# Kernel optimization log

Measured on AMD Instinct MI355X. Metric: run time of the kernel, lower is better.

The kernel has to match this reference:

```python
import jax, jax.numpy as jnp
import numpy as np

STATE_DIM = 512
N_AGENTS = 16
N_ACTIONS = 32
EMBED = 512          # mixing_embed_dim
Q_IN = STATE_DIM + N_AGENTS * N_ACTIONS  # 1024 (coma_critic arch)
ROWS = 32768         # bs * ts = 64 * 512


def _linear_params(key, d_in, d_out):
    kw, kb = jax.random.split(key)
    bound = 1.0 / np.sqrt(d_in)
    W = jax.random.uniform(kw, (d_in, d_out), minval=-bound, maxval=bound, dtype=jnp.float32)
    b = jax.random.uniform(kb, (d_out,), minval=-bound, maxval=bound, dtype=jnp.float32)
    return W, b


def setup_inputs() -> dict:
    key = jax.random.key(0)
    ks = jax.random.split(key, 8)
    states = jax.random.normal(ks[0], (ROWS, STATE_DIM), dtype=jnp.float32)
    actions = jax.random.uniform(ks[1], (ROWS, N_AGENTS * N_ACTIONS), dtype=jnp.float32)
    Qw1, Qb1 = _linear_params(ks[2], Q_IN, EMBED)
    Qw2, Qb2 = _linear_params(ks[3], EMBED, EMBED)
    Qw3, Qb3 = _linear_params(ks[4], EMBED, 1)
    Vw1, Vb1 = _linear_params(ks[5], STATE_DIM, EMBED)
    Vw2, Vb2 = _linear_params(ks[6], EMBED, EMBED)
    Vw3, Vb3 = _linear_params(ks[7], EMBED, 1)
    return {
        "states": states, "actions": actions,
        "Qw1": Qw1, "Qb1": Qb1, "Qw2": Qw2, "Qb2": Qb2, "Qw3": Qw3, "Qb3": Qb3,
        "Vw1": Vw1, "Vb1": Vb1, "Vw2": Vw2, "Vb2": Vb2, "Vw3": Vw3, "Vb3": Vb3,
    }


def _mlp3(x, W1, b1, W2, b2, W3, b3):
    h = jax.nn.relu(x @ W1 + b1)
    h = jax.nn.relu(h @ W2 + b2)
    return h @ W3 + b3


def reference(states, actions,
              Qw1, Qb1, Qw2, Qb2, Qw3, Qb3,
              Vw1, Vb1, Vw2, Vb2, Vw3, Vb3):
    # coma_critic arch: inputs = cat([states, joint-action one-hots], dim=1)
    inputs = jnp.concatenate([states, actions], axis=1)  # [bs*ts, Q_IN]
    q_outputs = _mlp3(inputs, Qw1, Qb1, Qw2, Qb2, Qw3, Qb3)  # [bs*ts, 1]
    v_outputs = _mlp3(states, Vw1, Vb1, Vw2, Vb2, Vw3, Vb3)  # [bs*ts, 1]
    return q_outputs, v_outputs
```

## Files before the change

### kernel.cpp

```cpp
#include <hip/hip_runtime.h>


#define ROWS 32768
#define EMBED 512

using frag_ab = __attribute__((ext_vector_type(8))) short;
using f32x4   = __attribute__((ext_vector_type(4))) float;

__device__ __forceinline__ unsigned short f2bf(float f) {
    unsigned int u = __builtin_bit_cast(unsigned int, f);
    return (unsigned short)((u + 0x7fffu + ((u >> 16) & 1u)) >> 16);
}

__device__ __forceinline__ unsigned pk2rne(float lo, float hi) {
    return (unsigned)f2bf(lo) | ((unsigned)f2bf(hi) << 16);
}

__device__ __forceinline__ void async_copy16(const void* g, void* l) {
    __builtin_amdgcn_global_load_lds(
        (const __attribute__((address_space(1))) unsigned int*)g,
        (__attribute__((address_space(3))) unsigned int*)l, 16, 0, 0);
}

#define VM0()   asm volatile("s_waitcnt vmcnt(0)" ::: "memory")
#define LGKM0() asm volatile("s_waitcnt lgkmcnt(0)" ::: "memory")
#define SBAR()  __builtin_amdgcn_s_barrier()
#define SCHED0() __builtin_amdgcn_sched_barrier(0)

__global__ __launch_bounds__(256)
void prep(const float* __restrict__ states, const float* __restrict__ actions,
          const float* __restrict__ Qw1, const float* __restrict__ Qw2,
          const float* __restrict__ Vw1, const float* __restrict__ Vw2,
          const float* __restrict__ qb3, const float* __restrict__ vb3,
          unsigned short* __restrict__ X,
          unsigned short* __restrict__ Qw1t, unsigned short* __restrict__ Qw2t,
          unsigned short* __restrict__ Vw1t, unsigned short* __restrict__ Vw2t,
          float* __restrict__ out) {
    const int b = blockIdx.x, tid = threadIdx.x;
    if (b < 4096) {
        int c = b * 256 + tid;
        int m = c >> 5, col = (c & 31) * 32;
        const float* src = (col < 512) ? states + (size_t)m * 512 + col
                                       : actions + (size_t)m * 512 + (col - 512);
        float4 f[8];
#pragma unroll
        for (int i = 0; i < 8; i++) f[i] = ((const float4*)src)[i];
        uint4* dst = (uint4*)(X + (size_t)m * 1024 + col);
#pragma unroll
        for (int i = 0; i < 4; i++)
            dst[i] = make_uint4(pk2rne(f[2*i].x,   f[2*i].y),
                                pk2rne(f[2*i].z,   f[2*i].w),
                                pk2rne(f[2*i+1].x, f[2*i+1].y),
                                pk2rne(f[2*i+1].z, f[2*i+1].w));
    } else if (b < 4416) {
        __shared__ float T[64][65];
        int tg = b - 4096;
        const float* W; unsigned short* O; int Krows, kt, nt;
        if (tg < 128) { W = Qw1; O = Qw1t; Krows = 1024; kt = tg >> 3; nt = tg & 7; }
        else {
            tg -= 128; int seg = tg >> 6, r = tg & 63;
            kt = r >> 3; nt = r & 7; Krows = 512;
            W = (seg == 0) ? Qw2 : (seg == 1) ? Vw1 : Vw2;
            O = (seg == 0) ? Qw2t : (seg == 1) ? Vw1t : Vw2t;
        }
        const int k0 = kt * 64, n0 = nt * 64;
        const int rr = tid >> 4, c4 = (tid & 15) * 4;
#pragma unroll
        for (int p = 0; p < 4; ++p) {
            float4 v = *(const float4*)&W[(size_t)(k0 + p * 16 + rr) * 512 + n0 + c4];
            T[p * 16 + rr][c4]     = v.x;
            T[p * 16 + rr][c4 + 1] = v.y;
            T[p * 16 + rr][c4 + 2] = v.z;
            T[p * 16 + rr][c4 + 3] = v.w;
        }
        __syncthreads();
        const int n = tid >> 2, kc = (tid & 3) * 16;
        unsigned pk[8];
#pragma unroll
        for (int j = 0; j < 8; ++j)
            pk[j] = pk2rne(T[kc + 2 * j][n], T[kc + 2 * j + 1][n]);
        uint4* dst = (uint4*)(O + (size_t)(n0 + n) * Krows + k0 + kc);
        dst[0] = make_uint4(pk[0], pk[1], pk[2], pk[3]);
        dst[1] = make_uint4(pk[4], pk[5], pk[6], pk[7]);
    } else {
        int i = (b - 4416) * 256 + tid;
        out[i] = (i < ROWS) ? qb3[0] : vb3[0];
    }
}

__device__ __forceinline__ void gemm_256(
    const unsigned short* __restrict__ A, int ldaE,
    const unsigned short* __restrict__ Bt, int ldbE,
    int K, int bm, int bn, char* smb, f32x4 acc[8][4])
{
    const int tid = threadIdx.x, wave = tid >> 6, lane = tid & 63;
    const int im = wave >> 2, in = wave & 3;
    const int lrow = lane & 15, quad = lane >> 4;
    const int ldaB = ldaE * 2, ldbB = ldbE * 2;

    const int srow = wave * 8 + (lane >> 3);
    const int scol = (((lane & 7) ^ ((lane >> 3) & 7)) << 4);
    const char* gA = (const char*)A + (size_t)(bm + srow) * ldaB + scol;
    const char* gB = (const char*)Bt + (size_t)(bn + srow) * ldbB + scol;
    char* ldsAw = smb + wave * 1024;
    char* ldsBw = smb + 65536 + wave * 1024;

    auto stageA = [&](int b, int h) {
        const char* g = gA + (size_t)(h * 128) * ldaB;
        char* l = ldsAw + b * 32768 + h * 16384;
        async_copy16(g, l);
        async_copy16(g + (size_t)64 * ldaB, l + 8192);
    };
    auto stageB = [&](int b, int h) {
        const char* g = gB + (size_t)(h * 128) * ldbB;
        char* l = ldsBw + b * 32768 + h * 16384;
        async_copy16(g, l);
        async_copy16(g + (size_t)64 * ldbB, l + 8192);
    };

    frag_ab a[4][2], b0[2][2], b1[2][2];

    auto readA = [&](int b, int mh) {
        const char* base = smb + b * 32768 + im * 16384;
#pragma unroll
        for (int i = 0; i < 4; ++i) {
            const int r = mh * 64 + i * 16 + lrow;
#pragma unroll
            for (int s = 0; s < 2; ++s)
                a[i][s] = *(const frag_ab*)(base + r * 128 +
                              (((s * 4 + quad) ^ (r & 7)) << 4));
        }
    };
    auto readB = [&](int b, int nh, frag_ab bb[2][2]) {
#pragma unroll
        for (int j = 0; j < 2; ++j) {
            const int nr = in * 64 + nh * 32 + j * 16 + lrow;
            const char* base = smb + 65536 + b * 32768 + (nr >> 7) * 16384;
            const int r = nr & 127;
#pragma unroll
            for (int s = 0; s < 2; ++s)
                bb[j][s] = *(const frag_ab*)(base + r * 128 +
                               (((s * 4 + quad) ^ (r & 7)) << 4));
        }
    };
    auto mma = [&](int mh, int nh, frag_ab bb[2][2]) {
        __builtin_amdgcn_s_setprio(1);
#pragma unroll
        for (int s = 0; s < 2; ++s)
#pragma unroll
            for (int i = 0; i < 4; ++i)
#pragma unroll
                for (int j = 0; j < 2; ++j)
                    acc[mh * 4 + i][nh * 2 + j] =
                        __builtin_amdgcn_mfma_f32_16x16x32_bf16(
                            a[i][s], bb[j][s], acc[mh * 4 + i][nh * 2 + j],
                            0, 0, 0);
        __builtin_amdgcn_s_setprio(0);
    };

    stageA(0, 0); stageB(0, 0); stageB(0, 1); stageA(0, 1);
    gA += 128; gB += 128;
    VM0();
    SBAR();

    const int NT = K >> 6;
    int buf = 0;
    for (int t = 0; t < NT; ++t) {
        const bool more = (t + 1 < NT);
        const int nb = buf ^ 1;
        readA(buf, 0); readB(buf, 0, b0);
        if (more) { stageA(nb, 0); stageB(nb, 0); }
        SBAR(); LGKM0(); SCHED0();
        mma(0, 0, b0);
        SBAR();
        readB(buf, 1, b1);
        if (more) stageB(nb, 1);
        SBAR(); LGKM0(); SCHED0();
        mma(0, 1, b1);
        SBAR();
        readA(buf, 1);
        if (more) { stageA(nb, 1); gA += 128; gB += 128; }
        SBAR(); LGKM0(); SCHED0();
        mma(1, 1, b1);
        SBAR();
        SBAR(); LGKM0(); SCHED0();
        mma(1, 0, b0);
        if (more) VM0();
        SBAR();
        buf ^= 1;
    }
}

__device__ __forceinline__ void decode_work(int bid, int& mi, int& v) {
    int work = ((bid & 7) << 6) | (bid >> 3);
    mi = work >> 2; v = work & 3;
}

__global__ __launch_bounds__(512, 2)
void layer1(const unsigned short* __restrict__ X,
            const unsigned short* __restrict__ Qw1t,
            const unsigned short* __restrict__ Vw1t,
            const float* __restrict__ Qb1, const float* __restrict__ Vb1,
            unsigned short* __restrict__ h1Q, unsigned short* __restrict__ h1V) {
    __shared__ __align__(16) char smem[131072];
    int mi, v; decode_work(blockIdx.x, mi, v);
    const bool isV = v >= 2;
    const int bm = mi * 256, bn = (v & 1) * 256;
    const int K = isV ? 512 : 1024;
    const unsigned short* Wt = isV ? Vw1t : Qw1t;
    const float* bias = isV ? Vb1 : Qb1;
    unsigned short* H = isV ? h1V : h1Q;

    f32x4 acc[8][4] = {};
    gemm_256(X, 1024, Wt, K, K, bm, bn, smem, acc);

    const int tid = threadIdx.x, wave = tid >> 6, lane = tid & 63;
    const int im = wave >> 2, in = wave & 3;
    const int lrow = lane & 15, quad = lane >> 4;
#pragma unroll
    for (int j = 0; j < 4; ++j) {
        const int col = bn + in * 64 + j * 16 + lrow;
        const float bc = bias[col];
#pragma unroll
        for (int i = 0; i < 8; ++i) {
            const int row0 = bm + im * 128 + i * 16 + quad * 4;
#pragma unroll
            for (int r = 0; r < 4; ++r) {
                float val = acc[i][j][r] + bc;
                val = val > 0.0f ? val : 0.0f;
                H[(size_t)(row0 + r) * EMBED + col] = f2bf(val);
            }
        }
    }
}

__global__ __launch_bounds__(512, 2)
void layer2(const unsigned short* __restrict__ h1Q,
            const unsigned short* __restrict__ h1V,
            const unsigned short* __restrict__ Qw2t,
            const unsigned short* __restrict__ Vw2t,
            const float* __restrict__ Qb2, const float* __restrict__ Vb2,
            const float* __restrict__ Qw3, const float* __restrict__ Vw3,
            float* __restrict__ out) {
    __shared__ __align__(16) char smem[131072];
    int mi, v; decode_work(blockIdx.x, mi, v);
    const bool isV = v >= 2;
    const int bm = mi * 256, bn = (v & 1) * 256;
    const unsigned short* A  = isV ? h1V : h1Q;
    const unsigned short* Wt = isV ? Vw2t : Qw2t;
    const float* bias = isV ? Vb2 : Qb2;
    const float* w3   = isV ? Vw3 : Qw3;
    float* op = out + (isV ? ROWS : 0);

    f32x4 acc[8][4] = {};
    gemm_256(A, 512, Wt, 512, 512, bm, bn, smem, acc);

    const int tid = threadIdx.x, wave = tid >> 6, lane = tid & 63;
    const int im = wave >> 2, in = wave & 3;
    const int lrow = lane & 15, quad = lane >> 4;
    float bc[4], wc[4];
#pragma unroll
    for (int j = 0; j < 4; ++j) {
        const int col = bn + in * 64 + j * 16 + lrow;
        bc[j] = bias[col];
        wc[j] = w3[col];
    }
#pragma unroll
    for (int i = 0; i < 8; ++i) {
#pragma unroll
        for (int r = 0; r < 4; ++r) {
            float s = 0.0f;
#pragma unroll
            for (int j = 0; j < 4; ++j) {
                float val = acc[i][j][r] + bc[j];
                val = val > 0.0f ? val : 0.0f;
                s += val * wc[j];
            }
#pragma unroll
            for (int m = 1; m < 16; m <<= 1) s += __shfl_xor(s, m, 64);
            if (lrow == 0)
                atomicAdd(&op[bm + im * 128 + i * 16 + quad * 4 + r], s);
        }
    }
}

extern "C" void kernel_launch(void* const* d_in, const int* in_sizes, int n_in,
                              void* d_out, int out_size, void* d_ws, size_t ws_size,
                              hipStream_t stream) {
    const float* states  = (const float*)d_in[0];
    const float* actions = (const float*)d_in[1];
    const float* Qw1 = (const float*)d_in[2];
    const float* Qb1 = (const float*)d_in[3];
    const float* Qw2 = (const float*)d_in[4];
    const float* Qb2 = (const float*)d_in[5];
    const float* Qw3 = (const float*)d_in[6];
    const float* Qb3 = (const float*)d_in[7];
    const float* Vw1 = (const float*)d_in[8];
    const float* Vb1 = (const float*)d_in[9];
    const float* Vw2 = (const float*)d_in[10];
    const float* Vb2 = (const float*)d_in[11];
    const float* Vw3 = (const float*)d_in[12];
    const float* Vb3 = (const float*)d_in[13];
    float* out = (float*)d_out;

    char* ws = (char*)d_ws;
    unsigned short* X    = (unsigned short*)ws;
    unsigned short* h1Q  = (unsigned short*)(ws + 67108864);
    unsigned short* h1V  = (unsigned short*)(ws + 100663296);
    unsigned short* Qw1t = (unsigned short*)(ws + 134217728);
    unsigned short* Qw2t = Qw1t + 512 * 1024;
    unsigned short* Vw1t = Qw2t + 512 * 512;
    unsigned short* Vw2t = Vw1t + 512 * 512;

    prep<<<dim3(4672), dim3(256), 0, stream>>>(states, actions, Qw1, Qw2, Vw1, Vw2,
                                               Qb3, Vb3, X, Qw1t, Qw2t, Vw1t, Vw2t, out);

    layer1<<<dim3(512), dim3(512), 0, stream>>>(X, Qw1t, Vw1t, Qb1, Vb1, h1Q, h1V);
    layer2<<<dim3(512), dim3(512), 0, stream>>>(h1Q, h1V, Qw2t, Vw2t, Qb2, Vb2, Qw3, Vw3, out);
}
```

Measured before the change: 289.6 us.

## Restructure GEMM main loop to prefetch two tiles ahead with partial vmcnt waits

The GEMM inner loop moves from a fine-grained schedule, with several barriers and lgkmcnt waits interleaving staged half-tiles, to a simpler double-buffer scheme. Both buffers are staged up front, the loop waits with vmcnt(8) so only the current tile must have landed, runs all four MMA blocks back to back, then refills the just-consumed buffer two tiles ahead. Separately, the prep conversion kernel now has each thread handle 8 elements instead of 32, with four times as many blocks, to raise memory parallelism. The goal is fewer barriers and more load latency hidden behind compute. The cost is less interleaving of LDS reads with MFMAs within an iteration.

```diff
diff --git a/kernel.cpp b/kernel.cpp
--- a/kernel.cpp
+++ b/kernel.cpp
@@ -22,10 +22,9 @@
         (__attribute__((address_space(3))) unsigned int*)l, 16, 0, 0);
 }
 
+#define VM8()   asm volatile("s_waitcnt vmcnt(8)" ::: "memory")
 #define VM0()   asm volatile("s_waitcnt vmcnt(0)" ::: "memory")
-#define LGKM0() asm volatile("s_waitcnt lgkmcnt(0)" ::: "memory")
 #define SBAR()  __builtin_amdgcn_s_barrier()
-#define SCHED0() __builtin_amdgcn_sched_barrier(0)
 
 __global__ __launch_bounds__(256)
 void prep(const float* __restrict__ states, const float* __restrict__ actions,
@@ -37,24 +36,19 @@
           unsigned short* __restrict__ Vw1t, unsigned short* __restrict__ Vw2t,
           float* __restrict__ out) {
     const int b = blockIdx.x, tid = threadIdx.x;
-    if (b < 4096) {
-        int c = b * 256 + tid;
-        int m = c >> 5, col = (c & 31) * 32;
+    if (b < 16384) {
+        int g = b * 256 + tid;
+        int m = g >> 7, col = (g & 127) * 8;
         const float* src = (col < 512) ? states + (size_t)m * 512 + col
                                        : actions + (size_t)m * 512 + (col - 512);
-        float4 f[8];
-#pragma unroll
-        for (int i = 0; i < 8; i++) f[i] = ((const float4*)src)[i];
-        uint4* dst = (uint4*)(X + (size_t)m * 1024 + col);
-#pragma unroll
-        for (int i = 0; i < 4; i++)
-            dst[i] = make_uint4(pk2rne(f[2*i].x,   f[2*i].y),
-                                pk2rne(f[2*i].z,   f[2*i].w),
-                                pk2rne(f[2*i+1].x, f[2*i+1].y),
-                                pk2rne(f[2*i+1].z, f[2*i+1].w));
-    } else if (b < 4416) {
+        float4 f0 = ((const float4*)src)[0];
+        float4 f1 = ((const float4*)src)[1];
+        *(uint4*)(X + (size_t)m * 1024 + col) =
+            make_uint4(pk2rne(f0.x, f0.y), pk2rne(f0.z, f0.w),
+                       pk2rne(f1.x, f1.y), pk2rne(f1.z, f1.w));
+    } else if (b < 16704) {
         __shared__ float T[64][65];
-        int tg = b - 4096;
+        int tg = b - 16384;
         const float* W; unsigned short* O; int Krows, kt, nt;
         if (tg < 128) { W = Qw1; O = Qw1t; Krows = 1024; kt = tg >> 3; nt = tg & 7; }
         else {
@@ -83,7 +77,7 @@
         dst[0] = make_uint4(pk[0], pk[1], pk[2], pk[3]);
         dst[1] = make_uint4(pk[4], pk[5], pk[6], pk[7]);
     } else {
-        int i = (b - 4416) * 256 + tid;
+        int i = (b - 16704) * 256 + tid;
         out[i] = (i < ROWS) ? qb3[0] : vb3[0];
     }
 }
@@ -105,17 +99,22 @@
     char* ldsAw = smb + wave * 1024;
     char* ldsBw = smb + 65536 + wave * 1024;
 
-    auto stageA = [&](int b, int h) {
-        const char* g = gA + (size_t)(h * 128) * ldaB;
-        char* l = ldsAw + b * 32768 + h * 16384;
-        async_copy16(g, l);
-        async_copy16(g + (size_t)64 * ldaB, l + 8192);
-    };
-    auto stageB = [&](int b, int h) {
-        const char* g = gB + (size_t)(h * 128) * ldbB;
-        char* l = ldsBw + b * 32768 + h * 16384;
-        async_copy16(g, l);
-        async_copy16(g + (size_t)64 * ldbB, l + 8192);
+    auto stageTile = [&](int b) {
+#pragma unroll
+        for (int h = 0; h < 2; ++h) {
+            const char* g = gA + (size_t)(h * 128) * ldaB;
+            char* l = ldsAw + b * 32768 + h * 16384;
+            async_copy16(g, l);
+            async_copy16(g + (size_t)64 * ldaB, l + 8192);
+        }
+#pragma unroll
+        for (int h = 0; h < 2; ++h) {
+            const char* g = gB + (size_t)(h * 128) * ldbB;
+            char* l = ldsBw + b * 32768 + h * 16384;
+            async_copy16(g, l);
+            async_copy16(g + (size_t)64 * ldbB, l + 8192);
+        }
+        gA += 128; gB += 128;
     };
 
     frag_ab a[4][2], b0[2][2], b1[2][2];
@@ -158,35 +157,23 @@
         __builtin_amdgcn_s_setprio(0);
     };
 
-    stageA(0, 0); stageB(0, 0); stageB(0, 1); stageA(0, 1);
-    gA += 128; gB += 128;
-    VM0();
-    SBAR();
+    stageTile(0);
+    stageTile(1);
 
     const int NT = K >> 6;
     int buf = 0;
     for (int t = 0; t < NT; ++t) {
-        const bool more = (t + 1 < NT);
-        const int nb = buf ^ 1;
+        if (t + 1 < NT) VM8(); else VM0();
+        SBAR();
         readA(buf, 0); readB(buf, 0, b0);
-        if (more) { stageA(nb, 0); stageB(nb, 0); }
-        SBAR(); LGKM0(); SCHED0();
         mma(0, 0, b0);
+        readB(buf, 1, b1);
+        mma(0, 1, b1);
+        readA(buf, 1);
+        mma(1, 1, b1);
+        mma(1, 0, b0);
         SBAR();
-        readB(buf, 1, b1);
-        if (more) stageB(nb, 1);
-        SBAR(); LGKM0(); SCHED0();
-        mma(0, 1, b1);
-        SBAR();
-        readA(buf, 1);
-        if (more) { stageA(nb, 1); gA += 128; gB += 128; }
-        SBAR(); LGKM0(); SCHED0();
-        mma(1, 1, b1);
-        SBAR();
-        SBAR(); LGKM0(); SCHED0();
-        mma(1, 0, b0);
-        if (more) VM0();
-        SBAR();
+        if (t + 2 < NT) stageTile(buf);
         buf ^= 1;
     }
 }
@@ -312,8 +299,8 @@
     unsigned short* Vw1t = Qw2t + 512 * 512;
     unsigned short* Vw2t = Vw1t + 512 * 512;
 
-    prep<<<dim3(4672), dim3(256), 0, stream>>>(states, actions, Qw1, Qw2, Vw1, Vw2,
-                                               Qb3, Vb3, X, Qw1t, Qw2t, Vw1t, Vw2t, out);
+    prep<<<dim3(16960), dim3(256), 0, stream>>>(states, actions, Qw1, Qw2, Vw1, Vw2,
+                                                Qb3, Vb3, X, Qw1t, Qw2t, Vw1t, Vw2t, out);
 
     layer1<<<dim3(512), dim3(512), 0, stream>>>(X, Qw1t, Vw1t, Qb1, Vb1, h1Q, h1V);
     layer2<<<dim3(512), dim3(512), 0, stream>>>(h1Q, h1V, Qw2t, Vw2t, Qb2, Vb2, Qw3, Vw3, out);
```

Result: faster. 283.0 us (-2.3%).
